# Kernel tuning notes

Hardware: AMD Instinct MI355X
Metric: run time of the kernel (lower is better)

## Reference

```python
import jax, jax.numpy as jnp
import numpy as np

GROUPS = 8
EPS = 1e-5
V, CIN, COUT, K, TDIM, B = 49152, 128, 256, 8, 256, 1
E = V * 9


def group_norm(x, gamma, beta):
    # x: [B, V, C]; torch GroupNorm semantics: normalize over (pixels, channels-in-group)
    b, v, c = x.shape
    xg = x.reshape(b, v, GROUPS, c // GROUPS)
    mu = xg.mean(axis=(1, 3), keepdims=True)
    var = xg.var(axis=(1, 3), keepdims=True)
    xg = (xg - mu) * jax.lax.rsqrt(var + EPS)
    return xg.reshape(b, v, c) * gamma + beta


def cheb_conv(x, row, col, vals, w):
    # x: [B, V, C]; w: [K, C, F]; Chebyshev recurrence on sparse Laplacian
    b, v, c = x.shape
    k = w.shape[0]
    xt = x.transpose(1, 0, 2).reshape(v, b * c)  # [V, B*C]

    def spmv(z):  # sparse L @ z via scatter-add
        return jnp.zeros_like(z).at[row].add(vals[:, None] * z[col])

    terms = [xt]
    if k > 1:
        terms.append(spmv(xt))
    for _ in range(k - 2):
        terms.append(2.0 * spmv(terms[-1]) - terms[-2])
    t = jnp.stack(terms).reshape(k, v, b, c)  # [K, V, B, C]
    return jnp.einsum('kvbc,kcf->bvf', t, w)  # [B, V, F]


def setup_inputs() -> dict:
    key = jax.random.key(0)
    ks = jax.random.split(key, 12)
    return {
        'x': jax.random.normal(ks[0], (B, V, CIN), jnp.float32),
        'time_emb': jax.random.normal(ks[1], (B, TDIM), jnp.float32),
        'row': jax.random.randint(ks[2], (E,), 0, V),
        'col': jax.random.randint(ks[3], (E,), 0, V),
        'vals': jax.random.normal(ks[4], (E,), jnp.float32) * 0.1,
        'w_res': jax.random.normal(ks[5], (K, CIN, COUT), jnp.float32) * 0.05,
        'w1': jax.random.normal(ks[6], (K, CIN, COUT), jnp.float32) * 0.05,
        'w2': jax.random.normal(ks[7], (K, COUT, COUT), jnp.float32) * 0.05,
        'g1': jnp.ones((CIN,), jnp.float32),
        'b1': jnp.zeros((CIN,), jnp.float32),
        'g2': jnp.ones((COUT,), jnp.float32),
        'b2': jnp.zeros((COUT,), jnp.float32),
        'wt': jax.random.normal(ks[8], (TDIM, COUT), jnp.float32) * 0.05,
        'bt': jnp.zeros((COUT,), jnp.float32),
    }


def reference(x, time_emb, row, col, vals, w_res, w1, w2, g1, b1, g2, b2, wt, bt):
    # conv_res (in_channels != out_channels), pooling = identity
    res = cheb_conv(x, row, col, vals, w_res)
    # block1: conv(silu(group_norm(x)))
    h = cheb_conv(jax.nn.silu(group_norm(x, g1, b1)), row, col, vals, w1)
    # time embedding: SiLU -> Linear -> broadcast over pixels
    h = h + (jax.nn.silu(time_emb) @ wt + bt)[:, None, :]
    # block2
    h = cheb_conv(jax.nn.silu(group_norm(h, g2, b2)), row, col, vals, w2)
    return h + res
```

## Files before the change

### kernel.cpp

```cpp
#include <hip/hip_runtime.h>
#include <cstddef>

#define V_N 49152
#define E_N 442368
#define E_PAD 589824
#define GEPS 1e-5f
#define CO 256
#define TD 256

typedef _Float16 h16;
typedef _Float16 h8v __attribute__((ext_vector_type(8)));
typedef _Float16 h4v __attribute__((ext_vector_type(4)));
typedef float f4v __attribute__((ext_vector_type(4)));

__device__ __forceinline__ void gload_lds16(const void* g, void* l) {
    __builtin_amdgcn_global_load_lds(
        (const __attribute__((address_space(1))) unsigned int*)g,
        (__attribute__((address_space(3))) unsigned int*)l, 16, 0, 0);
}

__global__ void count_edges(const int* __restrict__ row, int* __restrict__ cnt) {
    int e = blockIdx.x * blockDim.x + threadIdx.x;
    if (e < E_N) atomicAdd(&cnt[row[e]], 1);
}

__global__ void scan_rowptr(int* __restrict__ cnt, int* __restrict__ rowptr) {
    __shared__ int part[1024];
    const int CHUNK = V_N / 1024;
    int t = threadIdx.x;
    int base = t * CHUNK;
    int s = 0;
    for (int i = 0; i < CHUNK; ++i) s += (cnt[base + i] + 3) & ~3;
    part[t] = s;
    __syncthreads();
    for (int off = 1; off < 1024; off <<= 1) {
        int v = part[t];
        int add = (t >= off) ? part[t - off] : 0;
        __syncthreads();
        part[t] = v + add;
        __syncthreads();
    }
    int run = (t == 0) ? 0 : part[t - 1];
    for (int i = 0; i < CHUNK; ++i) {
        int c = cnt[base + i];
        rowptr[base + i] = run;
        cnt[base + i] = run;
        run += (c + 3) & ~3;
    }
    if (t == 1023) rowptr[V_N] = run;
}

__global__ void fill_csr(const int* __restrict__ row, const int* __restrict__ col,
                         const float* __restrict__ vals, int* __restrict__ cursor,
                         int2* __restrict__ ep) {
    int e = blockIdx.x * blockDim.x + threadIdx.x;
    if (e < E_N) {
        int r = row[e];
        int slot = atomicAdd(&cursor[r], 1);
        ep[slot] = make_int2(col[e], __float_as_int(vals[e]));
    }
}

__global__ void wprep(const float* __restrict__ w, h16* __restrict__ wt, int KC) {
    __shared__ float t[16][17];
    int kc = blockIdx.x * 16 + threadIdx.y;
    int f = blockIdx.y * 16 + threadIdx.x;
    t[threadIdx.y][threadIdx.x] = w[(size_t)kc * CO + f];
    __syncthreads();
    int fo = blockIdx.y * 16 + threadIdx.y;
    int kco = blockIdx.x * 16 + threadIdx.x;
    wt[(size_t)fo * KC + kco] = (h16)t[threadIdx.x][threadIdx.y];
}

template <int C>
__global__ void gn_stats2(const float* __restrict__ x, const float* __restrict__ tvec,
                          float* __restrict__ part) {
    __shared__ float ls[8], lss[8];
    int t = threadIdx.x;
    if (t < 8) { ls[t] = 0.f; lss[t] = 0.f; }
    __syncthreads();
    const int total4 = V_N * (C / 4);
    const int cmask = (C / 4) - 1;
    const int stride = gridDim.x * blockDim.x;
    int i0 = blockIdx.x * blockDim.x + t;
    const int c4 = i0 & cmask;
    float t0 = 0.f, t1 = 0.f, t2 = 0.f, t3 = 0.f;
    if (tvec) {
        t0 = tvec[c4 * 4 + 0]; t1 = tvec[c4 * 4 + 1];
        t2 = tvec[c4 * 4 + 2]; t3 = tvec[c4 * 4 + 3];
    }
    float s = 0.f, ss = 0.f;
    for (int i = i0; i < total4; i += stride) {
        float4 v = ((const float4*)x)[i];
        v.x += t0; v.y += t1; v.z += t2; v.w += t3;
        s  += v.x + v.y + v.z + v.w;
        ss += v.x * v.x + v.y * v.y + v.z * v.z + v.w * v.w;
    }
    constexpr int GL = (C == 128) ? 4 : 8;
#pragma unroll
    for (int off = 1; off < GL; off <<= 1) {
        s  += __shfl_xor(s, off);
        ss += __shfl_xor(ss, off);
    }
    int lane = t & 63;
    if ((lane & (GL - 1)) == 0) {
        int g = c4 >> ((C == 128) ? 2 : 3);
        atomicAdd(&ls[g], s);
        atomicAdd(&lss[g], ss);
    }
    __syncthreads();
    if (t < 16) part[blockIdx.x * 16 + t] = (t < 8) ? ls[t] : lss[t - 8];
}

#define GN_BLOCKS 512

__global__ void gn_reduce(const float* __restrict__ part, float* __restrict__ stats,
                          int nb) {
    __shared__ float acc[16];
    int t = threadIdx.x;
    if (t < 16) acc[t] = 0.f;
    __syncthreads();
    int idx = t & 15;
    float s = 0.f;
    for (int j = t >> 4; j < nb; j += 16) s += part[j * 16 + idx];
    atomicAdd(&acc[idx], s);
    __syncthreads();
    if (t < 16) stats[t] = acc[t];
}

__global__ void gn1_apply(const float* __restrict__ x, const float* __restrict__ stats,
                          const float* __restrict__ gamma, const float* __restrict__ beta,
                          h16* __restrict__ dst, int ldT) {
    const float Ng = (float)V_N * 16.f;
    const int total4 = V_N * 32;
    for (int i = blockIdx.x * blockDim.x + threadIdx.x; i < total4;
         i += gridDim.x * blockDim.x) {
        int c4 = i & 31;
        int v = i >> 5;
        float4 xv = ((const float4*)x)[i];
        float in[4] = {xv.x, xv.y, xv.z, xv.w};
        h4v o, oc;
#pragma unroll
        for (int j = 0; j < 4; ++j) {
            int c = c4 * 4 + j;
            int g = c >> 4;
            float mu = stats[g] / Ng;
            float var = stats[8 + g] / Ng - mu * mu;
            float rs = rsqrtf(var + GEPS);
            float y = (in[j] - mu) * rs * gamma[c] + beta[c];
            y = y / (1.f + expf(-y));
            o[j] = (h16)y;
            oc[j] = (h16)in[j];
        }
        size_t base = (size_t)v * ldT + c4 * 4;
        *(h4v*)&dst[base] = o;
        *(h4v*)&dst[base + 128] = oc;
    }
}

__global__ void gn2_apply(const float* __restrict__ x, const float* __restrict__ tvec,
                          const float* __restrict__ stats, const float* __restrict__ gamma,
                          const float* __restrict__ beta, h16* __restrict__ dst, int ldT) {
    const float Ng = (float)V_N * 32.f;
    const int total4 = V_N * 64;
    for (int i = blockIdx.x * blockDim.x + threadIdx.x; i < total4;
         i += gridDim.x * blockDim.x) {
        int c4 = i & 63;
        int v = i >> 6;
        float4 xv = ((const float4*)x)[i];
        float in[4] = {xv.x, xv.y, xv.z, xv.w};
        h4v o;
#pragma unroll
        for (int j = 0; j < 4; ++j) {
            int c = c4 * 4 + j;
            int g = c >> 5;
            float mu = stats[g] / Ng;
            float var = stats[8 + g] / Ng - mu * mu;
            float rs = rsqrtf(var + GEPS);
            float val = in[j] + tvec[c];
            float y = (val - mu) * rs * gamma[c] + beta[c];
            y = y / (1.f + expf(-y));
            o[j] = (h16)y;
        }
        *(h4v*)&dst[(size_t)v * ldT + c4 * 4] = o;
    }
}

__global__ void time_mlp(const float* __restrict__ te, const float* __restrict__ wt,
                         const float* __restrict__ bt, float* __restrict__ tvec) {
    __shared__ float s[TD];
    int f = threadIdx.x;
    float v = te[f];
    s[f] = v / (1.f + expf(-v));
    __syncthreads();
    float acc = bt[f];
    for (int t = 0; t < TD; ++t) acc += s[t] * wt[t * CO + f];
    tvec[f] = acc;
}

template <bool RECUR>
__global__ void spmv2(const int* __restrict__ rowptr, const int2* __restrict__ ep,
                      const h16* __restrict__ zb, const h16* __restrict__ pb,
                      h16* __restrict__ db, int ldT) {
    int wid = threadIdx.x >> 6, lane = threadIdx.x & 63;
    int half = lane >> 5, hl = lane & 31;
    int v = blockIdx.x * 8 + wid * 2 + half;
    int s = rowptr[v], e = rowptr[v + 1];
    float acc[8];
#pragma unroll
    for (int i = 0; i < 8; ++i) acc[i] = 0.f;
    const int4* e4 = (const int4*)(ep + s);
    int n4 = (e - s) >> 1;
    for (int i = 0; i < n4; i += 2) {
        int4 a0 = e4[i], a1 = e4[i + 1];
        h8v z0 = *(const h8v*)&zb[(size_t)a0.x * ldT + hl * 8];
        h8v z1 = *(const h8v*)&zb[(size_t)a0.z * ldT + hl * 8];
        h8v z2 = *(const h8v*)&zb[(size_t)a1.x * ldT + hl * 8];
        h8v z3 = *(const h8v*)&zb[(size_t)a1.z * ldT + hl * 8];
        float v0 = __int_as_float(a0.y), v1 = __int_as_float(a0.w);
        float v2 = __int_as_float(a1.y), v3 = __int_as_float(a1.w);
#pragma unroll
        for (int k = 0; k < 8; ++k)
            acc[k] += v0 * (float)z0[k] + v1 * (float)z1[k] +
                      v2 * (float)z2[k] + v3 * (float)z3[k];
    }
    size_t base = (size_t)v * ldT + hl * 8;
    h8v o;
    if (RECUR) {
        h8v pv = *(const h8v*)&pb[base];
#pragma unroll
        for (int i = 0; i < 8; ++i) o[i] = (h16)(2.f * acc[i] - (float)pv[i]);
    } else {
#pragma unroll
        for (int i = 0; i < 8; ++i) o[i] = (h16)acc[i];
    }
    *(h8v*)&db[base] = o;
}

template <int MODE, bool DUAL>
__global__ __launch_bounds__(512, 4) void gemm_f16(
    const h16* __restrict__ A, int lda, const h16* __restrict__ Wt,
    const h16* __restrict__ Wt2, int ldw, int wofs, int KC, int ksh,
    const float* __restrict__ bias, float* __restrict__ out,
    float* __restrict__ out2) {
    __shared__ h16 As[3][64 * 32];
    __shared__ h16 Bs[3][256 * 32];
    if (DUAL && blockIdx.y) { A += 128; Wt = Wt2; out = out2; }
    const int tid = threadIdx.x;
    const int wid = tid >> 6, lane = tid & 63;
    const int m0 = blockIdx.x * 64;
    const int fr = lane & 15, fq = lane >> 4;
    const int rl = lane >> 2;
    const int qs = (lane & 3) ^ ((lane >> 3) & 3);
    const int kmsk = (1 << ksh) - 1;
    const h16* Wb = Wt + wofs;
    const h16* Arow = A + (size_t)(m0 + wid * 16 + rl) * lda;
    const h16* Wrow = Wb + (size_t)(wid * 32 + rl) * ldw;

    f4v acc[4][2];
#pragma unroll
    for (int i = 0; i < 4; ++i)
#pragma unroll
        for (int n = 0; n < 2; ++n) acc[i][n] = (f4v){0.f, 0.f, 0.f, 0.f};

    const int nt = KC >> 5;
    auto stage = [&](int t, int buf) {
        int kk = t << 5;
        int ca = (((kk >> ksh) << 8) | (kk & kmsk)) + qs * 8;
        int cb = kk + qs * 8;
        if (wid < 4) gload_lds16(Arow + ca, &As[buf][(wid * 16) * 32]);
#pragma unroll
        for (int j = 0; j < 2; ++j)
            gload_lds16(Wrow + (size_t)(j * 16) * ldw + cb,
                        &Bs[buf][(wid * 32 + j * 16) * 32]);
    };
    stage(0, 0);
    stage(1, 1);
    stage(2, 2);

    const int slot = (fq ^ ((fr >> 1) & 3)) * 8;
    int cur = 0;
    for (int t = 0; t < nt; ++t) {
        if (wid < 4) asm volatile("s_waitcnt vmcnt(6)" ::: "memory");
        else         asm volatile("s_waitcnt vmcnt(4)" ::: "memory");
        __builtin_amdgcn_s_barrier();
        __builtin_amdgcn_sched_barrier(0);
        h8v af[4], bf[2];
#pragma unroll
        for (int i = 0; i < 4; ++i)
            af[i] = *(const h8v*)&As[cur][(i * 16 + fr) * 32 + slot];
#pragma unroll
        for (int n = 0; n < 2; ++n)
            bf[n] = *(const h8v*)&Bs[cur][(wid * 32 + n * 16 + fr) * 32 + slot];
        __builtin_amdgcn_s_setprio(1);
#pragma unroll
        for (int i = 0; i < 4; ++i)
#pragma unroll
            for (int n = 0; n < 2; ++n)
                acc[i][n] = __builtin_amdgcn_mfma_f32_16x16x32_f16(af[i], bf[n],
                                                                   acc[i][n], 0, 0, 0);
        __builtin_amdgcn_s_setprio(0);
        __builtin_amdgcn_sched_barrier(0);
        __builtin_amdgcn_s_barrier();
        if (t + 3 < nt) stage(t + 3, cur);
        cur = (cur == 2) ? 0 : cur + 1;
    }
#pragma unroll
    for (int i = 0; i < 4; ++i)
#pragma unroll
        for (int n = 0; n < 2; ++n)
#pragma unroll
            for (int rr = 0; rr < 4; ++rr) {
                int row = m0 + i * 16 + fq * 4 + rr;
                int col = wid * 32 + n * 16 + fr;
                size_t idx = (size_t)row * CO + col;
                if (MODE == 0) out[idx] = acc[i][n][rr];
                else if (MODE == 1) out[idx] += acc[i][n][rr];
                else out[idx] = bias[idx] + acc[i][n][rr];
            }
}

static void chain_spmv(hipStream_t s, int chunk, int k0, int kend, h16* terms, int ldT,
                       const int* rp, const int2* ep) {
    for (int k = (k0 == 0 ? 1 : k0); k < kend; ++k) {
        const h16* zb = terms + ((k - 1) % chunk) * 256;
        h16* db = terms + (k % chunk) * 256;
        if (k == 1) {
            spmv2<false><<<V_N / 8, 256, 0, s>>>(rp, ep, zb, nullptr, db, ldT);
        } else {
            const h16* pb = terms + ((k - 2) % chunk) * 256;
            spmv2<true><<<V_N / 8, 256, 0, s>>>(rp, ep, zb, pb, db, ldT);
        }
    }
}

extern "C" void kernel_launch(void* const* d_in, const int* in_sizes, int n_in,
                              void* d_out, int out_size, void* d_ws, size_t ws_size,
                              hipStream_t stream) {
    const float* x    = (const float*)d_in[0];
    const float* te   = (const float*)d_in[1];
    const int*   row  = (const int*)d_in[2];
    const int*   col  = (const int*)d_in[3];
    const float* vals = (const float*)d_in[4];
    const float* wres = (const float*)d_in[5];
    const float* w1   = (const float*)d_in[6];
    const float* w2   = (const float*)d_in[7];
    const float* g1   = (const float*)d_in[8];
    const float* b1   = (const float*)d_in[9];
    const float* g2   = (const float*)d_in[10];
    const float* b2   = (const float*)d_in[11];
    const float* wt   = (const float*)d_in[12];
    const float* bt   = (const float*)d_in[13];
    float* out = (float*)d_out;

    const size_t slot_b = (size_t)V_N * 256 * 2;
    const size_t res_b  = (size_t)V_N * 256 * 4;
    const size_t csr_b  = (size_t)(V_N + V_N + 1) * 4 + (size_t)E_PAD * 8;
    const size_t wt_b   = (size_t)(1024 + 2048 + 1024) * CO * 2;
    const size_t misc_b = 8192 + (size_t)GN_BLOCKS * 16 * 4;
    auto need = [&](int ch) { return (size_t)ch * slot_b + res_b + csr_b + wt_b + misc_b; };
    int chunk = (ws_size >= need(8)) ? 8 : (ws_size >= need(4)) ? 4 : 2;
    if (ws_size < need(2)) return;
    const int ldT = chunk * 256;

    char* p = (char*)d_ws;
    h16* terms = (h16*)p;              p += (size_t)chunk * slot_b;
    float* resbuf = (float*)p;         p += res_b;
    h16* w1t = (h16*)p;                p += (size_t)1024 * CO * 2;
    h16* w2t = (h16*)p;                p += (size_t)2048 * CO * 2;
    h16* wrt = (h16*)p;                p += (size_t)1024 * CO * 2;
    int* cnt = (int*)p;                p += (size_t)V_N * 4;
    int* rp  = (int*)p;                p += (size_t)(V_N + 1) * 4;
    int2* ep = (int2*)p;               p += (size_t)E_PAD * 8;
    float* stats = (float*)p;          p += 64;
    float* tv = (float*)p;             p += 1024;
    float* gpart = (float*)p;          p += (size_t)GN_BLOCKS * 16 * 4;

    hipMemsetAsync(cnt, 0, V_N * sizeof(int), stream);
    hipMemsetAsync(ep, 0, (size_t)E_PAD * 8, stream);
    count_edges<<<E_N / 256, 256, 0, stream>>>(row, cnt);
    scan_rowptr<<<1, 1024, 0, stream>>>(cnt, rp);
    fill_csr<<<E_N / 256, 256, 0, stream>>>(row, col, vals, cnt, ep);

    wprep<<<dim3(1024 / 16, 16), dim3(16, 16), 0, stream>>>(w1, w1t, 1024);
    wprep<<<dim3(2048 / 16, 16), dim3(16, 16), 0, stream>>>(w2, w2t, 2048);
    wprep<<<dim3(1024 / 16, 16), dim3(16, 16), 0, stream>>>(wres, wrt, 1024);

    time_mlp<<<1, 256, 0, stream>>>(te, wt, bt, tv);

    gn_stats2<128><<<GN_BLOCKS, 256, 0, stream>>>(x, nullptr, gpart);
    gn_reduce<<<1, 256, 0, stream>>>(gpart, stats, GN_BLOCKS);
    gn1_apply<<<2048, 256, 0, stream>>>(x, stats, g1, b1, terms, ldT);

    for (int k0 = 0; k0 < 8; k0 += chunk) {
        int kend = (k0 + chunk < 8) ? k0 + chunk : 8;
        chain_spmv(stream, chunk, k0, kend, terms, ldT, rp, ep);
        int KC = (kend - k0) * 128;
        dim3 g(V_N / 64, 2);
        if (k0 == 0)
            gemm_f16<0, true><<<g, 512, 0, stream>>>(terms, ldT, w1t, wrt, 1024,
                                                     k0 * 128, KC, 7, nullptr, out, resbuf);
        else
            gemm_f16<1, true><<<g, 512, 0, stream>>>(terms, ldT, w1t, wrt, 1024,
                                                     k0 * 128, KC, 7, nullptr, out, resbuf);
    }

    gn_stats2<256><<<GN_BLOCKS, 256, 0, stream>>>(out, tv, gpart);
    gn_reduce<<<1, 256, 0, stream>>>(gpart, stats, GN_BLOCKS);
    gn2_apply<<<2048, 256, 0, stream>>>(out, tv, stats, g2, b2, terms, ldT);

    for (int k0 = 0; k0 < 8; k0 += chunk) {
        int kend = (k0 + chunk < 8) ? k0 + chunk : 8;
        chain_spmv(stream, chunk, k0, kend, terms, ldT, rp, ep);
        int KC = (kend - k0) * 256;
        dim3 g(V_N / 64);
        if (k0 == 0)
            gemm_f16<2, false><<<g, 512, 0, stream>>>(terms, ldT, w2t, nullptr, 2048,
                                                      0, KC, 8, resbuf, out, nullptr);
        else
            gemm_f16<1, false><<<g, 512, 0, stream>>>(terms, ldT, w2t, nullptr, 2048,
                                                      k0 * 256, KC, 8, nullptr, out, nullptr);
    }
}
```

Baseline: 892.8 us.

## Split GEMM N into halves with 256-thread blocks, XCD-aware mapping, double buffering

The GEMM block now covers a 64x128 output tile with 4 waves instead of 64x256 with 8 waves, so twice as many blocks are launched. Block IDs are remapped so that consecutive M tiles stay on the same XCD. The three-stage LDS pipeline with manual vmcnt waits and priority hints is replaced by a simpler two-buffer prefetch using __syncthreads. This is meant to raise occupancy and L2 locality, but it reloads each A tile once per N half and makes the prefetch pipeline shallower.

```diff
diff --git a/kernel.cpp b/kernel.cpp
--- a/kernel.cpp
+++ b/kernel.cpp
@@ -238,24 +238,30 @@
 }
 
 template <int MODE, bool DUAL>
-__global__ __launch_bounds__(512, 4) void gemm_f16(
+__global__ __launch_bounds__(256, 6) void gemm_f16(
     const h16* __restrict__ A, int lda, const h16* __restrict__ Wt,
     const h16* __restrict__ Wt2, int ldw, int wofs, int KC, int ksh,
     const float* __restrict__ bias, float* __restrict__ out,
     float* __restrict__ out2) {
-    __shared__ h16 As[3][64 * 32];
-    __shared__ h16 Bs[3][256 * 32];
+    __shared__ h16 As[2][64 * 32];
+    __shared__ h16 Bs[2][128 * 32];
     if (DUAL && blockIdx.y) { A += 128; Wt = Wt2; out = out2; }
+    const int bid = blockIdx.x;
+    const int xcd = bid & 7;
+    const int j = bid >> 3;
+    const int mblk = xcd * 96 + (j >> 1);
+    const int nh = j & 1;
+    const int m0 = mblk * 64;
+    const int n0 = nh * 128;
     const int tid = threadIdx.x;
     const int wid = tid >> 6, lane = tid & 63;
-    const int m0 = blockIdx.x * 64;
     const int fr = lane & 15, fq = lane >> 4;
     const int rl = lane >> 2;
     const int qs = (lane & 3) ^ ((lane >> 3) & 3);
     const int kmsk = (1 << ksh) - 1;
     const h16* Wb = Wt + wofs;
     const h16* Arow = A + (size_t)(m0 + wid * 16 + rl) * lda;
-    const h16* Wrow = Wb + (size_t)(wid * 32 + rl) * ldw;
+    const h16* Wrow = Wb + (size_t)(n0 + wid * 32 + rl) * ldw;
 
     f4v acc[4][2];
 #pragma unroll
@@ -264,27 +270,18 @@
         for (int n = 0; n < 2; ++n) acc[i][n] = (f4v){0.f, 0.f, 0.f, 0.f};
 
     const int nt = KC >> 5;
-    auto stage = [&](int t, int buf) {
-        int kk = t << 5;
-        int ca = (((kk >> ksh) << 8) | (kk & kmsk)) + qs * 8;
-        int cb = kk + qs * 8;
-        if (wid < 4) gload_lds16(Arow + ca, &As[buf][(wid * 16) * 32]);
-#pragma unroll
-        for (int j = 0; j < 2; ++j)
-            gload_lds16(Wrow + (size_t)(j * 16) * ldw + cb,
-                        &Bs[buf][(wid * 32 + j * 16) * 32]);
-    };
-    stage(0, 0);
-    stage(1, 1);
-    stage(2, 2);
+    {
+        gload_lds16(Arow + qs * 8, &As[0][(wid * 16) * 32]);
+#pragma unroll
+        for (int j2 = 0; j2 < 2; ++j2)
+            gload_lds16(Wrow + (size_t)(j2 * 16) * ldw + qs * 8,
+                        &Bs[0][(wid * 32 + j2 * 16) * 32]);
+    }
+    __syncthreads();
 
     const int slot = (fq ^ ((fr >> 1) & 3)) * 8;
-    int cur = 0;
     for (int t = 0; t < nt; ++t) {
-        if (wid < 4) asm volatile("s_waitcnt vmcnt(6)" ::: "memory");
-        else         asm volatile("s_waitcnt vmcnt(4)" ::: "memory");
-        __builtin_amdgcn_s_barrier();
-        __builtin_amdgcn_sched_barrier(0);
+        const int cur = t & 1;
         h8v af[4], bf[2];
 #pragma unroll
         for (int i = 0; i < 4; ++i)
@@ -292,18 +289,24 @@
 #pragma unroll
         for (int n = 0; n < 2; ++n)
             bf[n] = *(const h8v*)&Bs[cur][(wid * 32 + n * 16 + fr) * 32 + slot];
-        __builtin_amdgcn_s_setprio(1);
+        if (t + 1 < nt) {
+            int kk = (t + 1) << 5;
+            int ca = (((kk >> ksh) << 8) | (kk & kmsk)) + qs * 8;
+            int cb = kk + qs * 8;
+            int nb = cur ^ 1;
+            gload_lds16(Arow + ca, &As[nb][(wid * 16) * 32]);
+#pragma unroll
+            for (int j2 = 0; j2 < 2; ++j2)
+                gload_lds16(Wrow + (size_t)(j2 * 16) * ldw + cb,
+                            &Bs[nb][(wid * 32 + j2 * 16) * 32]);
+        }
 #pragma unroll
         for (int i = 0; i < 4; ++i)
 #pragma unroll
             for (int n = 0; n < 2; ++n)
                 acc[i][n] = __builtin_amdgcn_mfma_f32_16x16x32_f16(af[i], bf[n],
                                                                    acc[i][n], 0, 0, 0);
-        __builtin_amdgcn_s_setprio(0);
-        __builtin_amdgcn_sched_barrier(0);
-        __builtin_amdgcn_s_barrier();
-        if (t + 3 < nt) stage(t + 3, cur);
-        cur = (cur == 2) ? 0 : cur + 1;
+        __syncthreads();
     }
 #pragma unroll
     for (int i = 0; i < 4; ++i)
@@ -312,7 +315,7 @@
 #pragma unroll
             for (int rr = 0; rr < 4; ++rr) {
                 int row = m0 + i * 16 + fq * 4 + rr;
-                int col = wid * 32 + n * 16 + fr;
+                int col = n0 + wid * 32 + n * 16 + fr;
                 size_t idx = (size_t)row * CO + col;
                 if (MODE == 0) out[idx] = acc[i][n][rr];
                 else if (MODE == 1) out[idx] += acc[i][n][rr];
@@ -396,12 +399,12 @@
         int kend = (k0 + chunk < 8) ? k0 + chunk : 8;
         chain_spmv(stream, chunk, k0, kend, terms, ldT, rp, ep);
         int KC = (kend - k0) * 128;
-        dim3 g(V_N / 64, 2);
+        dim3 g(V_N / 64 * 2, 2);
         if (k0 == 0)
-            gemm_f16<0, true><<<g, 512, 0, stream>>>(terms, ldT, w1t, wrt, 1024,
+            gemm_f16<0, true><<<g, 256, 0, stream>>>(terms, ldT, w1t, wrt, 1024,
                                                      k0 * 128, KC, 7, nullptr, out, resbuf);
         else
-            gemm_f16<1, true><<<g, 512, 0, stream>>>(terms, ldT, w1t, wrt, 1024,
+            gemm_f16<1, true><<<g, 256, 0, stream>>>(terms, ldT, w1t, wrt, 1024,
                                                      k0 * 128, KC, 7, nullptr, out, resbuf);
     }
 
@@ -413,12 +416,12 @@
         int kend = (k0 + chunk < 8) ? k0 + chunk : 8;
         chain_spmv(stream, chunk, k0, kend, terms, ldT, rp, ep);
         int KC = (kend - k0) * 256;
-        dim3 g(V_N / 64);
+        dim3 g(V_N / 64 * 2);
         if (k0 == 0)
-            gemm_f16<2, false><<<g, 512, 0, stream>>>(terms, ldT, w2t, nullptr, 2048,
+            gemm_f16<2, false><<<g, 256, 0, stream>>>(terms, ldT, w2t, nullptr, 2048,
                                                       0, KC, 8, resbuf, out, nullptr);
         else
-            gemm_f16<1, false><<<g, 512, 0, stream>>>(terms, ldT, w2t, nullptr, 2048,
+            gemm_f16<1, false><<<g, 256, 0, stream>>>(terms, ldT, w2t, nullptr, 2048,
                                                       k0 * 256, KC, 8, nullptr, out, nullptr);
     }
 }
```

Result: faster. 874.6 us (-2.0%).
